# Kernel optimization log

Measured on AMD Instinct MI355X. Metric: run time of the kernel, lower is better.

## Reference

```python
import jax, jax.numpy as jnp
import numpy as np

B, D, T = 8, 1024, 4096
Q, K, CD = 8, 1024, 32
COMMIT = 0.25
EPS = 1e-12


def setup_inputs() -> dict:
    key = jax.random.key(0)
    ks = jax.random.split(key, 6)
    x = jax.random.normal(ks[0], (B, D, T), dtype=jnp.float32)
    # stacked per-quantizer params: in_proj (1x1 conv == linear), out_proj, codebook
    Win = jax.random.normal(ks[1], (Q, CD, D), dtype=jnp.float32) * (1.0 / np.sqrt(D))
    b_in = jnp.zeros((Q, CD), dtype=jnp.float32)
    Wout = jax.random.normal(ks[2], (Q, D, CD), dtype=jnp.float32) * (1.0 / np.sqrt(CD))
    b_out = jnp.zeros((Q, D), dtype=jnp.float32)
    codebooks = jax.random.normal(ks[3], (Q, K, CD), dtype=jnp.float32)
    return {"x": x, "Win": Win, "b_in": b_in, "Wout": Wout, "b_out": b_out, "codebooks": codebooks}


def _l2norm(v):
    return v * jax.lax.rsqrt(jnp.sum(v * v, axis=-1, keepdims=True) + EPS)


def reference(x, Win, b_in, Wout, b_out, codebooks):
    """Residual VQ: sequential chain of factorized VQ layers.
    x: [B, D, T]. Returns (quantized_out [B,D,T], indices [Q,B,T], losses [Q]).
    """
    def step(residual, params):
        wi, bi, wo, bo, cb = params
        # in_proj: 1x1 conv == linear over channel dim
        z_e = jnp.einsum('bdt,cd->bct', residual, wi) + bi[None, :, None]  # [B,CD,T]
        enc = z_e.transpose(0, 2, 1).reshape(-1, z_e.shape[1])            # [B*T, CD]
        enc_n = _l2norm(enc)
        cb_n = _l2norm(cb)
        # full cdist^2 (argmin-equivalent, faithful to torch code)
        dist = (jnp.sum(enc_n * enc_n, -1, keepdims=True)
                - 2.0 * enc_n @ cb_n.T
                + jnp.sum(cb_n * cb_n, -1)[None, :])                       # [B*T, K]
        idx = jnp.argmin(dist, axis=-1).reshape(residual.shape[0], -1)     # [B, T]
        z_q = cb[idx].transpose(0, 2, 1)                                   # [B,CD,T]
        commit = jnp.mean((z_e - jax.lax.stop_gradient(z_q)) ** 2, axis=(1, 2))
        cbl = jnp.mean((z_q - jax.lax.stop_gradient(z_e)) ** 2, axis=(1, 2))
        loss = jnp.mean(COMMIT * commit + cbl)
        # straight-through estimator
        z_q = z_e + jax.lax.stop_gradient(z_q - z_e)
        q = jnp.einsum('bct,dc->bdt', z_q, wo) + bo[None, :, None]         # [B,D,T]
        return residual - q, (q, idx, loss)

    _, (qs, idxs, losses) = jax.lax.scan(step, x, (Win, b_in, Wout, b_out, codebooks))
    quantized_out = jnp.sum(qs, axis=0)
    return quantized_out, idxs, losses
```

## Files before the change

### kernel.cpp

```cpp
#include <hip/hip_runtime.h>
#include <math.h>

#define B 8
#define D 1024
#define T 4096
#define Q 8
#define K 1024
#define CD 32
#define BT (B * T)

#define OFF_Z0   ((size_t)0)
#define OFF_MT   (OFF_Z0 + (size_t)Q * B * CD * T * 8)
#define OFF_CBN  (OFF_MT + (size_t)64 * K * CD * 8)
#define OFF_N264 (OFF_CBN + (size_t)Q * K * CD * 8)
#define OFF_NT   (OFF_N264 + (size_t)Q * K * 8)
#define OFF_BEFF (OFF_NT + (size_t)64 * CD * CD * 8)
#define OFF_C32  (OFF_BEFF + (size_t)Q * CD * 8)
#define OFF_N232 (OFF_C32 + (size_t)Q * K * CD * 4)
#define OFF_W64  (OFF_N232 + (size_t)Q * K * 4)

__global__ void k_zero_losses(float* __restrict__ loss) {
    if (threadIdx.x < Q) loss[threadIdx.x] = 0.0f;
}

__global__ __launch_bounds__(256) void k_norm(const float* __restrict__ cb,
                                              double* __restrict__ cbn64,
                                              double* __restrict__ n264,
                                              float* __restrict__ cbn32,
                                              float* __restrict__ n232) {
    int i = blockIdx.x * 256 + threadIdx.x;
    const float* c = cb + (size_t)i * CD;
    double v[CD];
    double ss = 0.0;
#pragma unroll
    for (int j = 0; j < CD; ++j) { v[j] = (double)c[j]; ss += v[j] * v[j]; }
    double s = 1.0 / sqrt(ss + 1e-12);
    double n2 = 0.0;
    double* o = cbn64 + (size_t)i * CD;
    float* o32 = cbn32 + (size_t)i * CD;
#pragma unroll
    for (int j = 0; j < CD; ++j) {
        double vn = v[j] * s;
        o[j] = vn; o32[j] = (float)vn; n2 += vn * vn;
    }
    n264[i] = n2; n232[i] = (float)n2;
}

__global__ __launch_bounds__(256) void k_cvtW(const float* __restrict__ Win,
                                              double* __restrict__ Win64) {
    int i = blockIdx.x * 256 + threadIdx.x;
    Win64[i] = (double)Win[i];
}

__global__ __launch_bounds__(256) void k_prep_N(const float* __restrict__ Win,
                                                const float* __restrict__ Wout,
                                                double* __restrict__ Ntab) {
    const int q = blockIdx.x >> 3, j = blockIdx.x & 7;
    __shared__ float a_sh[CD][128];
    __shared__ float b_sh[128][CD];
    double acc[4] = {0.0, 0.0, 0.0, 0.0};
    for (int d0 = 0; d0 < D; d0 += 128) {
        __syncthreads();
        for (int i = threadIdx.x; i < CD * 128; i += 256) {
            int cc = i >> 7, dl = i & 127;
            a_sh[cc][dl] = Win[((size_t)q * CD + cc) * D + d0 + dl];
        }
        for (int i = threadIdx.x; i < 128 * CD; i += 256) {
            int dl = i >> 5, cc = i & 31;
            b_sh[dl][cc] = Wout[((size_t)j * D + d0 + dl) * CD + cc];
        }
        __syncthreads();
        for (int dl = 0; dl < 128; ++dl) {
#pragma unroll
            for (int r = 0; r < 4; ++r) {
                int i = r * 256 + threadIdx.x;
                acc[r] = fma((double)a_sh[i >> 5][dl], (double)b_sh[dl][i & 31], acc[r]);
            }
        }
    }
#pragma unroll
    for (int r = 0; r < 4; ++r) {
        int i = r * 256 + threadIdx.x;
        Ntab[((size_t)(q * 8 + j) * CD + (i >> 5)) * CD + (i & 31)] = acc[r];
    }
}

__global__ __launch_bounds__(256) void k_prep_M(const float* __restrict__ cb,
                                                const double* __restrict__ Ntab,
                                                double* __restrict__ Mt) {
    const int q = blockIdx.z, j = blockIdx.y;
    const int k = blockIdx.x * 256 + threadIdx.x;
    __shared__ double nsh[CD][CD];
    for (int i = threadIdx.x; i < CD * CD; i += 256)
        nsh[i >> 5][i & 31] = Ntab[(size_t)(q * 8 + j) * CD * CD + i];
    __syncthreads();
    double cv[CD];
    const float* cr = cb + ((size_t)j * K + k) * CD;
#pragma unroll
    for (int c = 0; c < CD; ++c) cv[c] = (double)cr[c];
    double* mo = Mt + (((size_t)(q * 8 + j) * K + k) * CD);
#pragma unroll
    for (int c = 0; c < CD; ++c) {
        double a = 0.0;
#pragma unroll
        for (int cp = 0; cp < CD; ++cp) a = fma(nsh[c][cp], cv[cp], a);
        mo[c] = a;
    }
}

__global__ __launch_bounds__(256) void k_prep_beff(const float* __restrict__ Win,
                                                   const float* __restrict__ b_in,
                                                   const float* __restrict__ b_out,
                                                   double* __restrict__ beff) {
    const int c = blockIdx.x, q = blockIdx.y;
    __shared__ double red[256];
    double p = 0.0;
    for (int d = threadIdx.x; d < D; d += 256) {
        double bp = 0.0;
        for (int j = 0; j < q; ++j) bp += (double)b_out[j * D + d];
        p = fma((double)Win[((size_t)q * CD + c) * D + d], bp, p);
    }
    red[threadIdx.x] = p;
    __syncthreads();
    for (int s = 128; s > 0; s >>= 1) {
        if (threadIdx.x < s) red[threadIdx.x] += red[threadIdx.x + s];
        __syncthreads();
    }
    if (threadIdx.x == 0) beff[q * CD + c] = (double)b_in[q * CD + c] - red[0];
}

__global__ __launch_bounds__(256) void k_gemmZ(const float* __restrict__ x,
                                               const double* __restrict__ Win64,
                                               const double* __restrict__ beff,
                                               double* __restrict__ z0) {
    int h = blockIdx.x;
    int u = h >> 3, r = h & 7;
    int q = u & 7;
    int m = r + 8 * (u >> 3);
    int b = m >> 4;
    int tc = m & 15;
    int t = tc * 256 + threadIdx.x;

    const double* w = Win64 + (size_t)q * CD * D;
    const double* be = beff + q * CD;
    const float* xb = x + (size_t)b * D * T + t;

    double acc[CD];
#pragma unroll
    for (int c = 0; c < CD; ++c) acc[c] = be[c];

    for (int d0 = 0; d0 < D; d0 += 8) {
        double xv[8];
#pragma unroll
        for (int i = 0; i < 8; ++i) xv[i] = (double)xb[(size_t)(d0 + i) * T];
#pragma unroll
        for (int c = 0; c < CD; ++c) {
            const double* wc = w + (size_t)c * D + d0;
#pragma unroll
            for (int i = 0; i < 8; ++i) acc[c] = fma(wc[i], xv[i], acc[c]);
        }
    }
    double* zo = z0 + (((size_t)q * B + b) * CD) * T + t;
#pragma unroll
    for (int c = 0; c < CD; ++c) zo[(size_t)c * T] = acc[c];
}

#define INS4(dd, ii)                                                           \
    do {                                                                       \
        float _d = (dd); int _i = (ii);                                        \
        if (_d < d4) {                                                         \
            d4 = _d; i4 = _i;                                                  \
            if (d4 < d3) { float tf = d3; d3 = d4; d4 = tf; int ti = i3; i3 = i4; i4 = ti; } \
            if (d3 < d2) { float tf = d2; d2 = d3; d3 = tf; int ti = i2; i2 = i3; i3 = ti; } \
            if (d2 < d1) { float tf = d1; d1 = d2; d2 = tf; int ti = i1; i1 = i2; i2 = ti; } \
        }                                                                      \
    } while (0)

#define AT 64
__global__ __launch_bounds__(1024) void k_argmin_fused(const double* __restrict__ z0,
                                                       const double* __restrict__ Mt,
                                                       const double* __restrict__ cbn64,
                                                       const double* __restrict__ n264,
                                                       const float* __restrict__ cbn32,
                                                       const float* __restrict__ n232,
                                                       const float* __restrict__ cb,
                                                       int* __restrict__ idxi,
                                                       float* __restrict__ idx_f,
                                                       float* __restrict__ loss) {
    const int lane = threadIdx.x & 63;
    const int wv = threadIdx.x >> 6;
    const int kcw = __builtin_amdgcn_readfirstlane(wv);
    const int t = blockIdx.x * AT + lane;
    const int b = blockIdx.y;
    const size_t bt = (size_t)b * T + t;

    __shared__ double zn_s[CD][AT];
    __shared__ float  znf_s[CD][AT];
    __shared__ float  a2_s[AT];
    __shared__ double rn_s[AT];
    __shared__ float  sd[16][4][AT];
    __shared__ int    si[16][4][AT];
    __shared__ int    hist_s[Q][AT];

    for (int q = 0; q < Q; ++q) {
        {
            const int c0 = wv * 2;
            double v0 = z0[(((size_t)q * B + b) * CD + c0) * T + t];
            double v1 = z0[(((size_t)q * B + b) * CD + c0 + 1) * T + t];
            for (int j = 0; j < q; ++j) {
                int kj = hist_s[j][lane];
                const double* m = Mt + (((size_t)(q * 8 + j) * K + kj) * CD);
                v0 -= m[c0];
                v1 -= m[c0 + 1];
            }
            zn_s[c0][lane] = v0;
            zn_s[c0 + 1][lane] = v1;
        }
        __syncthreads();

        if (wv == 0) {
            double ss = 0.0;
#pragma unroll
            for (int c = 0; c < CD; ++c) { double v = zn_s[c][lane]; ss += v * v; }
            double rnorm = sqrt(ss + 1e-12);
            double s = 1.0 / rnorm;
            float a2 = 0.0f;
#pragma unroll
            for (int c = 0; c < CD; ++c) {
                double vn = zn_s[c][lane] * s;
                zn_s[c][lane] = vn;
                float zf = (float)vn;
                znf_s[c][lane] = zf;
                a2 = fmaf(zf, zf, a2);
            }
            a2_s[lane] = a2;
            rn_s[lane] = rnorm;
        }
        __syncthreads();

        {
            float znf[CD];
#pragma unroll
            for (int c = 0; c < CD; ++c) znf[c] = znf_s[c][lane];
            const float a2 = a2_s[lane];

            float d1 = 1e30f, d2 = 1e30f, d3 = 1e30f, d4 = 1e30f;
            int i1 = 0, i2 = 0, i3 = 0, i4 = 0;
            const float4* cp = (const float4*)(cbn32 + ((size_t)q * K + (size_t)kcw * 64) * CD);
            const float* nq = n232 + q * K + kcw * 64;
            for (int k = 0; k < 64; k += 4) {
                const float4* c0 = cp + k * (CD / 4);
                float p0 = 0.f, p1 = 0.f, p2 = 0.f, p3 = 0.f;
                float r0 = 0.f, r1 = 0.f, r2 = 0.f, r3 = 0.f;
                float s0 = 0.f, s1 = 0.f, s2 = 0.f, s3 = 0.f;
                float u0 = 0.f, u1 = 0.f, u2 = 0.f, u3 = 0.f;
#pragma unroll
                for (int u = 0; u < CD / 4; ++u) {
                    float4 av = c0[u];
                    float4 bv = c0[u + 8];
                    float4 cv = c0[u + 16];
                    float4 dv = c0[u + 24];
                    float z0f = znf[u * 4 + 0], z1f = znf[u * 4 + 1];
                    float z2f = znf[u * 4 + 2], z3f = znf[u * 4 + 3];
                    p0 = fmaf(z0f, av.x, p0); p1 = fmaf(z1f, av.y, p1);
                    p2 = fmaf(z2f, av.z, p2); p3 = fmaf(z3f, av.w, p3);
                    r0 = fmaf(z0f, bv.x, r0); r1 = fmaf(z1f, bv.y, r1);
                    r2 = fmaf(z2f, bv.z, r2); r3 = fmaf(z3f, bv.w, r3);
                    s0 = fmaf(z0f, cv.x, s0); s1 = fmaf(z1f, cv.y, s1);
                    s2 = fmaf(z2f, cv.z, s2); s3 = fmaf(z3f, cv.w, s3);
                    u0 = fmaf(z0f, dv.x, u0); u1 = fmaf(z1f, dv.y, u1);
                    u2 = fmaf(z2f, dv.z, u2); u3 = fmaf(z3f, dv.w, u3);
                }
                float dist0 = fmaf(-2.0f, (p0 + p1) + (p2 + p3), a2) + nq[k];
                float dist1 = fmaf(-2.0f, (r0 + r1) + (r2 + r3), a2) + nq[k + 1];
                float dist2 = fmaf(-2.0f, (s0 + s1) + (s2 + s3), a2) + nq[k + 2];
                float dist3 = fmaf(-2.0f, (u0 + u1) + (u2 + u3), a2) + nq[k + 3];
                INS4(dist0, kcw * 64 + k);
                INS4(dist1, kcw * 64 + k + 1);
                INS4(dist2, kcw * 64 + k + 2);
                INS4(dist3, kcw * 64 + k + 3);
            }
            sd[wv][0][lane] = d1; sd[wv][1][lane] = d2;
            sd[wv][2][lane] = d3; sd[wv][3][lane] = d4;
            si[wv][0][lane] = i1; si[wv][1][lane] = i2;
            si[wv][2][lane] = i3; si[wv][3][lane] = i4;
        }
        __syncthreads();

        if (wv < 4) {
            float d1 = 1e30f, d2 = 1e30f, d3 = 1e30f, d4 = 1e30f;
            int i1 = 0, i2 = 0, i3 = 0, i4 = 0;
            for (int w = wv; w < 16; w += 4)
#pragma unroll
                for (int s4 = 0; s4 < 4; ++s4)
                    INS4(sd[w][s4][lane], si[w][s4][lane]);
            sd[wv][0][lane] = d1; sd[wv][1][lane] = d2;
            sd[wv][2][lane] = d3; sd[wv][3][lane] = d4;
            si[wv][0][lane] = i1; si[wv][1][lane] = i2;
            si[wv][2][lane] = i3; si[wv][3][lane] = i4;
        }
        __syncthreads();

        if (wv == 0) {
            float d1 = 1e30f, d2 = 1e30f, d3 = 1e30f, d4 = 1e30f;
            int i1 = 0, i2 = 0, i3 = 0, i4 = 0;
#pragma unroll
            for (int w = 0; w < 4; ++w)
#pragma unroll
                for (int s4 = 0; s4 < 4; ++s4)
                    INS4(sd[w][s4][lane], si[w][s4][lane]);

            const double rnorm = rn_s[lane];
            int bi;
            if (d4 - d1 >= 1e-4f) {
                int j1 = i1, j2 = i2, j3 = i3, j4 = i4;
                { int tt; if (j1 > j2) { tt = j1; j1 = j2; j2 = tt; }
                          if (j3 > j4) { tt = j3; j3 = j4; j4 = tt; }
                          if (j1 > j3) { tt = j1; j1 = j3; j3 = tt; }
                          if (j2 > j4) { tt = j2; j2 = j4; j4 = tt; }
                          if (j2 > j3) { tt = j2; j2 = j3; j3 = tt; } }
                const double* cq64 = cbn64 + (size_t)q * K * CD;
                const double* nq64 = n264 + (size_t)q * K;
                double dot1v = 0.0, dot2v = 0.0, dot3v = 0.0, dot4v = 0.0;
                double A = 0.0;
                const double* r1p = cq64 + (size_t)j1 * CD;
                const double* r2p = cq64 + (size_t)j2 * CD;
                const double* r3p = cq64 + (size_t)j3 * CD;
                const double* r4p = cq64 + (size_t)j4 * CD;
#pragma unroll
                for (int c = 0; c < CD; ++c) {
                    double vn = zn_s[c][lane];
                    A += vn * vn;
                    dot1v = fma(vn, r1p[c], dot1v);
                    dot2v = fma(vn, r2p[c], dot2v);
                    dot3v = fma(vn, r3p[c], dot3v);
                    dot4v = fma(vn, r4p[c], dot4v);
                }
                double e1 = (A - 2.0 * dot1v) + nq64[j1];
                double e2 = (A - 2.0 * dot2v) + nq64[j2];
                double e3 = (A - 2.0 * dot3v) + nq64[j3];
                double e4 = (A - 2.0 * dot4v) + nq64[j4];
                double best = e1; bi = j1;
                if (e2 < best) { best = e2; bi = j2; }
                if (e3 < best) { best = e3; bi = j3; }
                if (e4 < best) { best = e4; bi = j4; }
            } else {
                double zn[CD]; double A = 0.0;
#pragma unroll
                for (int c = 0; c < CD; ++c) { zn[c] = zn_s[c][lane]; A += zn[c] * zn[c]; }
                double best = 1e300; bi = 0;
                const double* cq64 = cbn64 + (size_t)q * K * CD;
                const double* nq64 = n264 + (size_t)q * K;
                for (int k = 0; k < K; k += 2) {
                    double dot0 = 0.0, dot1 = 0.0;
                    const double* c0 = cq64 + (size_t)k * CD;
                    const double* c1 = c0 + CD;
#pragma unroll
                    for (int c = 0; c < CD; ++c) {
                        dot0 = fma(zn[c], c0[c], dot0);
                        dot1 = fma(zn[c], c1[c], dot1);
                    }
                    double dist0 = (A - 2.0 * dot0) + nq64[k];
                    double dist1 = (A - 2.0 * dot1) + nq64[k + 1];
                    if (dist0 < best) { best = dist0; bi = k; }
                    if (dist1 < best) { best = dist1; bi = k + 1; }
                }
            }
            hist_s[q][lane] = bi;

            const float* cr = cb + ((size_t)q * K + bi) * CD;
            double sq = 0.0;
#pragma unroll
            for (int c = 0; c < CD; ++c) {
                double diff = zn_s[c][lane] * rnorm - (double)cr[c];
                sq = fma(diff, diff, sq);
            }
#pragma unroll
            for (int off = 32; off > 0; off >>= 1) sq += __shfl_down(sq, off);
            if (lane == 0)
                atomicAdd(&loss[q], (float)(sq * (1.25 / (double)((size_t)B * CD * T))));
            idxi[q * BT + bt] = bi;
            idx_f[(size_t)q * BT + bt] = (float)bi;
        }
        __syncthreads();
    }
}

#define GT 128
#define GD 128
__global__ __launch_bounds__(256) void k_gemm_final(const float* __restrict__ Wout,
                                                    const float* __restrict__ bo,
                                                    const float* __restrict__ cb,
                                                    const int* __restrict__ idxi,
                                                    float* __restrict__ out) {
    const int t0 = blockIdx.x * GT;
    const int b  = blockIdx.y;
    const int d0 = blockIdx.z * GD;
    const int tx = threadIdx.x & 15;
    const int ty = threadIdx.x >> 4;
    __shared__ float Wt[CD][GD + 4];
    __shared__ float Zt[CD][GT + 4];
    __shared__ float bsum[GD];

    if (threadIdx.x < GD) {
        float sjb = 0.0f;
#pragma unroll
        for (int j = 0; j < Q; ++j) sjb += bo[j * D + d0 + threadIdx.x];
        bsum[threadIdx.x] = sjb;
    }

    float acc[8][8];
#pragma unroll
    for (int r = 0; r < 8; ++r)
#pragma unroll
        for (int cc = 0; cc < 8; ++cc) acc[r][cc] = 0.0f;

    for (int j = 0; j < Q; ++j) {
        __syncthreads();
        for (int i = threadIdx.x; i < GD * CD; i += 256) {
            int dl = i >> 5, c = i & 31;
            Wt[c][dl] = Wout[((size_t)j * D + d0 + dl) * CD + c];
        }
        for (int i = threadIdx.x; i < GT * CD; i += 256) {
            int tl = i >> 5, c = i & 31;
            int kj = idxi[j * BT + (size_t)b * T + t0 + tl];
            Zt[c][tl] = cb[((size_t)j * K + kj) * CD + c];
        }
        __syncthreads();
#pragma unroll
        for (int k = 0; k < CD; ++k) {
            float a[8], zb[8];
            *(float4*)&a[0]  = *(const float4*)&Wt[k][ty * 8];
            *(float4*)&a[4]  = *(const float4*)&Wt[k][ty * 8 + 4];
            *(float4*)&zb[0] = *(const float4*)&Zt[k][tx * 8];
            *(float4*)&zb[4] = *(const float4*)&Zt[k][tx * 8 + 4];
#pragma unroll
            for (int r = 0; r < 8; ++r)
#pragma unroll
                for (int cc = 0; cc < 8; ++cc)
                    acc[r][cc] = fmaf(a[r], zb[cc], acc[r][cc]);
        }
    }
#pragma unroll
    for (int r = 0; r < 8; ++r) {
        const int d = d0 + ty * 8 + r;
        const float bias = bsum[ty * 8 + r];
        float4 v0, v1;
        v0.x = acc[r][0] + bias; v0.y = acc[r][1] + bias;
        v0.z = acc[r][2] + bias; v0.w = acc[r][3] + bias;
        v1.x = acc[r][4] + bias; v1.y = acc[r][5] + bias;
        v1.z = acc[r][6] + bias; v1.w = acc[r][7] + bias;
        float* op = out + ((size_t)b * D + d) * T + t0 + tx * 8;
        *(float4*)op = v0;
        *(float4*)(op + 4) = v1;
    }
}

extern "C" void kernel_launch(void* const* d_in, const int* in_sizes, int n_in,
                              void* d_out, int out_size, void* d_ws, size_t ws_size,
                              hipStream_t stream) {
    const float* x     = (const float*)d_in[0];
    const float* Win   = (const float*)d_in[1];
    const float* b_in  = (const float*)d_in[2];
    const float* Wout  = (const float*)d_in[3];
    const float* b_out = (const float*)d_in[4];
    const float* cb    = (const float*)d_in[5];

    float* out0  = (float*)d_out;
    float* idx_f = out0 + (size_t)B * D * T;
    float* loss  = idx_f + (size_t)Q * BT;

    char* sc = (char*)d_out;
    double* z0    = (double*)(sc + OFF_Z0);
    double* Mt    = (double*)(sc + OFF_MT);
    double* cbn64 = (double*)(sc + OFF_CBN);
    double* n264  = (double*)(sc + OFF_N264);
    double* Ntab  = (double*)(sc + OFF_NT);
    double* beff  = (double*)(sc + OFF_BEFF);
    float*  cbn32 = (float*)(sc + OFF_C32);
    float*  n232  = (float*)(sc + OFF_N232);
    double* Win64 = (double*)(sc + OFF_W64);
    int*    idxi  = (int*)d_ws;

    k_zero_losses<<<1, 64, 0, stream>>>(loss);
    k_norm<<<(Q * K) / 256, 256, 0, stream>>>(cb, cbn64, n264, cbn32, n232);
    k_cvtW<<<(Q * CD * D) / 256, 256, 0, stream>>>(Win, Win64);
    k_prep_N<<<64, 256, 0, stream>>>(Win, Wout, Ntab);
    k_prep_M<<<dim3(K / 256, 8, 8), 256, 0, stream>>>(cb, Ntab, Mt);
    k_prep_beff<<<dim3(CD, Q), 256, 0, stream>>>(Win, b_in, b_out, beff);

    k_gemmZ<<<Q * B * (T / 256), 256, 0, stream>>>(x, Win64, beff, z0);

    k_argmin_fused<<<dim3(T / AT, B), 1024, 0, stream>>>(z0, Mt, cbn64, n264,
                                                         cbn32, n232, cb,
                                                         idxi, idx_f, loss);

    k_gemm_final<<<dim3(T / GT, B, D / GD), 256, 0, stream>>>(Wout, b_out, cb, idxi, out0);
}
```

Baseline: 1.476 ms.

## Split gemmZ channels across blocks, packed FMA for argmin, parallelize rerank

The gemmZ kernel now splits the 32 output channels across two grid rows, halving accumulators per thread, and raises the occupancy hint. The fp32 candidate scoring in the argmin kernel uses packed v_pk_fma_f32 on paired z values read from shared memory instead of holding 32 floats in registers. The top-4 merge is done redundantly by four waves, and each computes one fp64 rerank distance in parallel instead of wave 0 doing all four. The changes target register pressure, occupancy and ALU throughput, but the gemmZ split rereads x twice and the rerank adds an extra shared array.

```diff
diff --git a/kernel.cpp b/kernel.cpp
--- a/kernel.cpp
+++ b/kernel.cpp
@@ -18,6 +18,16 @@
 #define OFF_C32  (OFF_BEFF + (size_t)Q * CD * 8)
 #define OFF_N232 (OFF_C32 + (size_t)Q * K * CD * 4)
 #define OFF_W64  (OFF_N232 + (size_t)Q * K * 4)
+
+typedef float f32x2 __attribute__((ext_vector_type(2)));
+
+__device__ __forceinline__ f32x2 mk2(float a, float b) { f32x2 r; r.x = a; r.y = b; return r; }
+
+__device__ __forceinline__ f32x2 pkfma(f32x2 a, f32x2 b, f32x2 c) {
+    f32x2 d;
+    asm("v_pk_fma_f32 %0, %1, %2, %3" : "=v"(d) : "v"(a), "v"(b), "v"(c));
+    return d;
+}
 
 __global__ void k_zero_losses(float* __restrict__ loss) {
     if (threadIdx.x < Q) loss[threadIdx.x] = 0.0f;
@@ -129,10 +139,10 @@
     if (threadIdx.x == 0) beff[q * CD + c] = (double)b_in[q * CD + c] - red[0];
 }
 
-__global__ __launch_bounds__(256) void k_gemmZ(const float* __restrict__ x,
-                                               const double* __restrict__ Win64,
-                                               const double* __restrict__ beff,
-                                               double* __restrict__ z0) {
+__global__ __launch_bounds__(256, 8) void k_gemmZ(const float* __restrict__ x,
+                                                  const double* __restrict__ Win64,
+                                                  const double* __restrict__ beff,
+                                                  double* __restrict__ z0) {
     int h = blockIdx.x;
     int u = h >> 3, r = h & 7;
     int q = u & 7;
@@ -140,29 +150,30 @@
     int b = m >> 4;
     int tc = m & 15;
     int t = tc * 256 + threadIdx.x;
-
-    const double* w = Win64 + (size_t)q * CD * D;
-    const double* be = beff + q * CD;
+    const int c0 = blockIdx.y * (CD / 2);
+
+    const double* w = Win64 + ((size_t)q * CD + c0) * D;
+    const double* be = beff + q * CD + c0;
     const float* xb = x + (size_t)b * D * T + t;
 
-    double acc[CD];
-#pragma unroll
-    for (int c = 0; c < CD; ++c) acc[c] = be[c];
+    double acc[CD / 2];
+#pragma unroll
+    for (int c = 0; c < CD / 2; ++c) acc[c] = be[c];
 
     for (int d0 = 0; d0 < D; d0 += 8) {
         double xv[8];
 #pragma unroll
         for (int i = 0; i < 8; ++i) xv[i] = (double)xb[(size_t)(d0 + i) * T];
 #pragma unroll
-        for (int c = 0; c < CD; ++c) {
+        for (int c = 0; c < CD / 2; ++c) {
             const double* wc = w + (size_t)c * D + d0;
 #pragma unroll
             for (int i = 0; i < 8; ++i) acc[c] = fma(wc[i], xv[i], acc[c]);
         }
     }
-    double* zo = z0 + (((size_t)q * B + b) * CD) * T + t;
-#pragma unroll
-    for (int c = 0; c < CD; ++c) zo[(size_t)c * T] = acc[c];
+    double* zo = z0 + (((size_t)q * B + b) * CD + c0) * T + t;
+#pragma unroll
+    for (int c = 0; c < CD / 2; ++c) zo[(size_t)c * T] = acc[c];
 }
 
 #define INS4(dd, ii)                                                           \
@@ -177,16 +188,16 @@
     } while (0)
 
 #define AT 64
-__global__ __launch_bounds__(1024) void k_argmin_fused(const double* __restrict__ z0,
-                                                       const double* __restrict__ Mt,
-                                                       const double* __restrict__ cbn64,
-                                                       const double* __restrict__ n264,
-                                                       const float* __restrict__ cbn32,
-                                                       const float* __restrict__ n232,
-                                                       const float* __restrict__ cb,
-                                                       int* __restrict__ idxi,
-                                                       float* __restrict__ idx_f,
-                                                       float* __restrict__ loss) {
+__global__ __launch_bounds__(1024, 8) void k_argmin_fused(const double* __restrict__ z0,
+                                                          const double* __restrict__ Mt,
+                                                          const double* __restrict__ cbn64,
+                                                          const double* __restrict__ n264,
+                                                          const float* __restrict__ cbn32,
+                                                          const float* __restrict__ n232,
+                                                          const float* __restrict__ cb,
+                                                          int* __restrict__ idxi,
+                                                          float* __restrict__ idx_f,
+                                                          float* __restrict__ loss) {
     const int lane = threadIdx.x & 63;
     const int wv = threadIdx.x >> 6;
     const int kcw = __builtin_amdgcn_readfirstlane(wv);
@@ -195,11 +206,12 @@
     const size_t bt = (size_t)b * T + t;
 
     __shared__ double zn_s[CD][AT];
-    __shared__ float  znf_s[CD][AT];
+    __shared__ f32x2  znf2_s[CD / 2][AT];
     __shared__ float  a2_s[AT];
     __shared__ double rn_s[AT];
     __shared__ float  sd[16][4][AT];
     __shared__ int    si[16][4][AT];
+    __shared__ double ed[4][AT];
     __shared__ int    hist_s[Q][AT];
 
     for (int q = 0; q < Q; ++q) {
@@ -225,56 +237,58 @@
             double rnorm = sqrt(ss + 1e-12);
             double s = 1.0 / rnorm;
             float a2 = 0.0f;
+            float zf_prev = 0.0f;
 #pragma unroll
             for (int c = 0; c < CD; ++c) {
                 double vn = zn_s[c][lane] * s;
                 zn_s[c][lane] = vn;
                 float zf = (float)vn;
-                znf_s[c][lane] = zf;
                 a2 = fmaf(zf, zf, a2);
+                if (c & 1) znf2_s[c >> 1][lane] = mk2(zf_prev, zf);
+                else zf_prev = zf;
             }
             a2_s[lane] = a2;
             rn_s[lane] = rnorm;
         }
         __syncthreads();
 
+        float d1 = 1e30f, d2 = 1e30f, d3 = 1e30f, d4 = 1e30f;
+        int i1 = 0, i2 = 0, i3 = 0, i4 = 0;
         {
-            float znf[CD];
-#pragma unroll
-            for (int c = 0; c < CD; ++c) znf[c] = znf_s[c][lane];
-            const float a2 = a2_s[lane];
-
-            float d1 = 1e30f, d2 = 1e30f, d3 = 1e30f, d4 = 1e30f;
-            int i1 = 0, i2 = 0, i3 = 0, i4 = 0;
+            const float a2v = a2_s[lane];
             const float4* cp = (const float4*)(cbn32 + ((size_t)q * K + (size_t)kcw * 64) * CD);
             const float* nq = n232 + q * K + kcw * 64;
             for (int k = 0; k < 64; k += 4) {
                 const float4* c0 = cp + k * (CD / 4);
-                float p0 = 0.f, p1 = 0.f, p2 = 0.f, p3 = 0.f;
-                float r0 = 0.f, r1 = 0.f, r2 = 0.f, r3 = 0.f;
-                float s0 = 0.f, s1 = 0.f, s2 = 0.f, s3 = 0.f;
-                float u0 = 0.f, u1 = 0.f, u2 = 0.f, u3 = 0.f;
+                f32x2 a0a = mk2(0.f, 0.f), a0b = mk2(0.f, 0.f);
+                f32x2 a1a = mk2(0.f, 0.f), a1b = mk2(0.f, 0.f);
+                f32x2 a2a = mk2(0.f, 0.f), a2b = mk2(0.f, 0.f);
+                f32x2 a3a = mk2(0.f, 0.f), a3b = mk2(0.f, 0.f);
 #pragma unroll
                 for (int u = 0; u < CD / 4; ++u) {
+                    f32x2 zpa = znf2_s[2 * u][lane];
+                    f32x2 zpb = znf2_s[2 * u + 1][lane];
                     float4 av = c0[u];
                     float4 bv = c0[u + 8];
                     float4 cv = c0[u + 16];
                     float4 dv = c0[u + 24];
-                    float z0f = znf[u * 4 + 0], z1f = znf[u * 4 + 1];
-                    float z2f = znf[u * 4 + 2], z3f = znf[u * 4 + 3];
-                    p0 = fmaf(z0f, av.x, p0); p1 = fmaf(z1f, av.y, p1);
-                    p2 = fmaf(z2f, av.z, p2); p3 = fmaf(z3f, av.w, p3);
-                    r0 = fmaf(z0f, bv.x, r0); r1 = fmaf(z1f, bv.y, r1);
-                    r2 = fmaf(z2f, bv.z, r2); r3 = fmaf(z3f, bv.w, r3);
-                    s0 = fmaf(z0f, cv.x, s0); s1 = fmaf(z1f, cv.y, s1);
-                    s2 = fmaf(z2f, cv.z, s2); s3 = fmaf(z3f, cv.w, s3);
-                    u0 = fmaf(z0f, dv.x, u0); u1 = fmaf(z1f, dv.y, u1);
-                    u2 = fmaf(z2f, dv.z, u2); u3 = fmaf(z3f, dv.w, u3);
+                    a0a = pkfma(zpa, mk2(av.x, av.y), a0a);
+                    a0b = pkfma(zpb, mk2(av.z, av.w), a0b);
+                    a1a = pkfma(zpa, mk2(bv.x, bv.y), a1a);
+                    a1b = pkfma(zpb, mk2(bv.z, bv.w), a1b);
+                    a2a = pkfma(zpa, mk2(cv.x, cv.y), a2a);
+                    a2b = pkfma(zpb, mk2(cv.z, cv.w), a2b);
+                    a3a = pkfma(zpa, mk2(dv.x, dv.y), a3a);
+                    a3b = pkfma(zpb, mk2(dv.z, dv.w), a3b);
                 }
-                float dist0 = fmaf(-2.0f, (p0 + p1) + (p2 + p3), a2) + nq[k];
-                float dist1 = fmaf(-2.0f, (r0 + r1) + (r2 + r3), a2) + nq[k + 1];
-                float dist2 = fmaf(-2.0f, (s0 + s1) + (s2 + s3), a2) + nq[k + 2];
-                float dist3 = fmaf(-2.0f, (u0 + u1) + (u2 + u3), a2) + nq[k + 3];
+                float dot0 = (a0a.x + a0b.x) + (a0a.y + a0b.y);
+                float dot1 = (a1a.x + a1b.x) + (a1a.y + a1b.y);
+                float dot2 = (a2a.x + a2b.x) + (a2a.y + a2b.y);
+                float dot3 = (a3a.x + a3b.x) + (a3a.y + a3b.y);
+                float dist0 = fmaf(-2.0f, dot0, a2v) + nq[k];
+                float dist1 = fmaf(-2.0f, dot1, a2v) + nq[k + 1];
+                float dist2 = fmaf(-2.0f, dot2, a2v) + nq[k + 2];
+                float dist3 = fmaf(-2.0f, dot3, a2v) + nq[k + 3];
                 INS4(dist0, kcw * 64 + k);
                 INS4(dist1, kcw * 64 + k + 1);
                 INS4(dist2, kcw * 64 + k + 2);
@@ -288,28 +302,34 @@
         __syncthreads();
 
         if (wv < 4) {
-            float d1 = 1e30f, d2 = 1e30f, d3 = 1e30f, d4 = 1e30f;
-            int i1 = 0, i2 = 0, i3 = 0, i4 = 0;
-            for (int w = wv; w < 16; w += 4)
+            d1 = d2 = d3 = d4 = 1e30f; i1 = i2 = i3 = i4 = 0;
+            for (int w = 0; w < 16; ++w)
 #pragma unroll
                 for (int s4 = 0; s4 < 4; ++s4)
                     INS4(sd[w][s4][lane], si[w][s4][lane]);
-            sd[wv][0][lane] = d1; sd[wv][1][lane] = d2;
-            sd[wv][2][lane] = d3; sd[wv][3][lane] = d4;
-            si[wv][0][lane] = i1; si[wv][1][lane] = i2;
-            si[wv][2][lane] = i3; si[wv][3][lane] = i4;
+
+            if (d4 - d1 >= 1e-4f) {
+                int j1 = i1, j2 = i2, j3 = i3, j4 = i4;
+                { int tt; if (j1 > j2) { tt = j1; j1 = j2; j2 = tt; }
+                          if (j3 > j4) { tt = j3; j3 = j4; j4 = tt; }
+                          if (j1 > j3) { tt = j1; j1 = j3; j3 = tt; }
+                          if (j2 > j4) { tt = j2; j2 = j4; j4 = tt; }
+                          if (j2 > j3) { tt = j2; j2 = j3; j3 = tt; } }
+                const int myj = (wv == 0) ? j1 : (wv == 1) ? j2 : (wv == 2) ? j3 : j4;
+                const double* cp64 = cbn64 + ((size_t)q * K + myj) * CD;
+                double A = 0.0, dot = 0.0;
+#pragma unroll
+                for (int c = 0; c < CD; ++c) {
+                    double vn = zn_s[c][lane];
+                    A += vn * vn;
+                    dot = fma(vn, cp64[c], dot);
+                }
+                ed[wv][lane] = (A - 2.0 * dot) + n264[(size_t)q * K + myj];
+            }
         }
         __syncthreads();
 
         if (wv == 0) {
-            float d1 = 1e30f, d2 = 1e30f, d3 = 1e30f, d4 = 1e30f;
-            int i1 = 0, i2 = 0, i3 = 0, i4 = 0;
-#pragma unroll
-            for (int w = 0; w < 4; ++w)
-#pragma unroll
-                for (int s4 = 0; s4 < 4; ++s4)
-                    INS4(sd[w][s4][lane], si[w][s4][lane]);
-
             const double rnorm = rn_s[lane];
             int bi;
             if (d4 - d1 >= 1e-4f) {
@@ -319,27 +339,8 @@
                           if (j1 > j3) { tt = j1; j1 = j3; j3 = tt; }
                           if (j2 > j4) { tt = j2; j2 = j4; j4 = tt; }
                           if (j2 > j3) { tt = j2; j2 = j3; j3 = tt; } }
-                const double* cq64 = cbn64 + (size_t)q * K * CD;
-                const double* nq64 = n264 + (size_t)q * K;
-                double dot1v = 0.0, dot2v = 0.0, dot3v = 0.0, dot4v = 0.0;
-                double A = 0.0;
-                const double* r1p = cq64 + (size_t)j1 * CD;
-                const double* r2p = cq64 + (size_t)j2 * CD;
-                const double* r3p = cq64 + (size_t)j3 * CD;
-                const double* r4p = cq64 + (size_t)j4 * CD;
-#pragma unroll
-                for (int c = 0; c < CD; ++c) {
-                    double vn = zn_s[c][lane];
-                    A += vn * vn;
-                    dot1v = fma(vn, r1p[c], dot1v);
-                    dot2v = fma(vn, r2p[c], dot2v);
-                    dot3v = fma(vn, r3p[c], dot3v);
-                    dot4v = fma(vn, r4p[c], dot4v);
-                }
-                double e1 = (A - 2.0 * dot1v) + nq64[j1];
-                double e2 = (A - 2.0 * dot2v) + nq64[j2];
-                double e3 = (A - 2.0 * dot3v) + nq64[j3];
-                double e4 = (A - 2.0 * dot4v) + nq64[j4];
+                double e1 = ed[0][lane], e2 = ed[1][lane];
+                double e3 = ed[2][lane], e4 = ed[3][lane];
                 double best = e1; bi = j1;
                 if (e2 < best) { best = e2; bi = j2; }
                 if (e3 < best) { best = e3; bi = j3; }
@@ -489,7 +490,7 @@
     k_prep_M<<<dim3(K / 256, 8, 8), 256, 0, stream>>>(cb, Ntab, Mt);
     k_prep_beff<<<dim3(CD, Q), 256, 0, stream>>>(Win, b_in, b_out, beff);
 
-    k_gemmZ<<<Q * B * (T / 256), 256, 0, stream>>>(x, Win64, beff, z0);
+    k_gemmZ<<<dim3(Q * B * (T / 256), 2), 256, 0, stream>>>(x, Win64, beff, z0);
 
     k_argmin_fused<<<dim3(T / AT, B), 1024, 0, stream>>>(z0, Mt, cbn64, n264,
                                                          cbn32, n232, cb,
```

After: 1.479 ms. Within noise of the previous version (+0.2%).
